# Kernel tuning notes

Hardware: AMD Instinct MI355X
Metric: run time of the kernel (lower is better)

The kernel has to match this reference:

```python
import jax, jax.numpy as jnp
import numpy as np
from jax import lax

ALPHA = 0.5
KERNEL = 25
NUM_P = 16
SEQ_LEN = 1440
PRED_LEN = 720
DWT_LEN = SEQ_LEN // 2 + 2            # 722 (pytorch_wavelets zero-mode, sym3 filt len 6)
FREQ = int(np.ceil(DWT_LEN / 2 * ALPHA) * 2)  # 362

_DEC_LO = np.array([0.035226291882100656, -0.08544127388224149, -0.13501102001039084,
                    0.4598775021193313, 0.8068915093133388, 0.3326705529509569], np.float32)
_DEC_HI = np.array([-0.3326705529509569, 0.8068915093133388, -0.4598775021193313,
                    -0.13501102001039084, 0.08544127388224149, 0.035226291882100656], np.float32)
DEC_LO, DEC_HI = jnp.asarray(_DEC_LO), jnp.asarray(_DEC_HI)
REC_LO, REC_HI = DEC_LO[::-1], DEC_HI[::-1]


def dwt1(x):
    # pytorch_wavelets DWT1DForward(J=1, mode='zero'): zero-pad then stride-2 true conv with dec filters
    B, C, L = x.shape
    out = (L + 5) // 2
    p = 2 * (out - 1) - L + 6
    xp = jnp.pad(x.reshape(B * C, 1, L), ((0, 0), (0, 0), (p // 2, p - p // 2)))
    ker = jnp.stack([DEC_LO[::-1], DEC_HI[::-1]])[:, None, :]   # (2,1,6); xcorr w/ reversed == conv
    y = lax.conv_general_dilated(xp, ker, (2,), 'VALID', dimension_numbers=('NCH', 'OIH', 'NCH'))
    return y[:, 0].reshape(B, C, out), y[:, 1].reshape(B, C, out)


def iwt1(lo, hi):
    # DWT1DInverse mode='zero': conv_transpose stride 2, padding L-2  ->  dilate + conv, pad 1
    B, C, n = lo.shape
    z = jnp.concatenate([lo.reshape(B * C, 1, n), hi.reshape(B * C, 1, n)], axis=1)
    ker = jnp.stack([REC_LO[::-1], REC_HI[::-1]])[None, :, :]   # (O=1, I=2, 6)
    y = lax.conv_general_dilated(z, ker, (1,), [(1, 1)], lhs_dilation=(2,),
                                 dimension_numbers=('NCH', 'OIH', 'NCH'))
    return y[:, 0].reshape(B, C, 2 * n - 4)


def mov_avg(x, k=KERNEL):
    pooled = lax.reduce_window(x, 0.0, lax.add, (1, 1, k), (1, 1, 1), 'VALID') / k
    return jnp.pad(pooled, ((0, 0), (0, 0), (k // 2, k // 2 - (k + 1) % 2)), mode='edge')


def mov_norm(x):
    mean = lax.stop_gradient(mov_avg(x))
    xc = lax.stop_gradient(x - mean)
    std = lax.stop_gradient(mov_avg(jnp.abs(xc))) + 1e-5
    return xc / std, mean, std


def inst_norm(x):
    mean = lax.stop_gradient(jnp.mean(x, -1, keepdims=True))
    xc = x - mean
    var = jnp.mean((xc - jnp.mean(xc, -1, keepdims=True)) ** 2, -1, keepdims=True)
    return xc / jnp.sqrt(var + 1e-5)


def mean_std_mlp(mean, std, mp, sp, mw1, mw2, sw1, sw2, mpred, spred):
    m_all = jnp.mean(mean, -1, keepdims=True)
    s_all = jnp.mean(std, -1, keepdims=True)
    mr = (mean - m_all) @ mp.T
    sr = (std - s_all) @ sp.T
    mr = jax.nn.relu(mr @ mw1.T) @ mw2.T
    sr = jax.nn.relu(sr @ sw1.T) @ sw2.T
    mean_o = mr @ mpred.T + m_all
    std_o = jax.nn.relu(sr @ spred.T + s_all) + 1e-5
    return mean_o, std_o


def forward(x, latent_w, latent_b, acp, dcp):
    xt = jnp.swapaxes(x, -1, 1)                    # (B, C, L)
    ac0, dc0 = dwt1(xt)                            # (B, C, DWT_LEN)
    ac_n = inst_norm(ac0)
    ac, m_ac, s_ac = mov_norm(ac0)
    dc, m_dc, s_dc = mov_norm(dc0)
    m_ac, s_ac = mean_std_mlp(m_ac, s_ac, *acp)    # MLPs[-1]
    m_dc, s_dc = mean_std_mlp(m_dc, s_dc, *dcp)    # MLPs[0]
    dcF = jnp.fft.fft(dc)
    acF = jnp.fft.fft(ac_n)
    idx = jnp.argsort(-jnp.abs(acF), axis=-1)[..., :FREQ]
    amp = ALPHA * jnp.take_along_axis(acF, idx, -1) + (1.0 - ALPHA) * jnp.take_along_axis(dcF, idx, -1)
    B, C, _ = dcF.shape
    bi = jnp.arange(B)[:, None, None]
    ci = jnp.arange(C)[None, :, None]
    dcF = dcF.at[bi, ci, idx].set(amp)
    dc = jnp.real(jnp.fft.ifft(dcF))
    xr = iwt1(ac, dc)                              # (B, C, SEQ_LEN)
    mean = iwt1(m_ac, m_dc)                        # (B, C, PRED_LEN)
    std = iwt1(s_ac, s_dc)
    xr = xr.reshape(B, C, NUM_P, SEQ_LEN // NUM_P)
    emb = xr @ latent_w.T + latent_b               # (B, C, NUM_P, d_model)
    return emb, mean, std


def setup_inputs() -> dict:
    key = jax.random.key(0)
    B, C = 64, 128
    d_model, d_ff = 512, 1024
    s = 0.02
    names_shapes = [
        ('x', (B, SEQ_LEN, C), 1.0),
        ('latent_w', (d_model, SEQ_LEN // NUM_P), s),
    ]
    for pre in ('ac', 'dc'):
        names_shapes += [
            (pre + '_mean_proj', (d_model, DWT_LEN), s),
            (pre + '_std_proj', (d_model, DWT_LEN), s),
            (pre + '_mean_ffn_w1', (d_ff, d_model), s),
            (pre + '_mean_ffn_w2', (d_model, d_ff), s),
            (pre + '_std_ffn_w1', (d_ff, d_model), s),
            (pre + '_std_ffn_w2', (d_model, d_ff), s),
            (pre + '_mean_pred', (PRED_LEN // 2 + 2, d_model), s),
            (pre + '_std_pred', (PRED_LEN // 2 + 2, d_model), s),
        ]
    keys = jax.random.split(key, len(names_shapes))
    inp = {n: jax.random.normal(k, shp, dtype=jnp.float32) * sc
           for (n, shp, sc), k in zip(names_shapes, keys)}
    inp['latent_b'] = jnp.zeros((d_model,), jnp.float32)
    return inp


def reference(x, latent_w, latent_b,
              ac_mean_proj, ac_std_proj, ac_mean_ffn_w1, ac_mean_ffn_w2,
              ac_std_ffn_w1, ac_std_ffn_w2, ac_mean_pred, ac_std_pred,
              dc_mean_proj, dc_std_proj, dc_mean_ffn_w1, dc_mean_ffn_w2,
              dc_std_ffn_w1, dc_std_ffn_w2, dc_mean_pred, dc_std_pred):
    acp = (ac_mean_proj, ac_std_proj, ac_mean_ffn_w1, ac_mean_ffn_w2,
           ac_std_ffn_w1, ac_std_ffn_w2, ac_mean_pred, ac_std_pred)
    dcp = (dc_mean_proj, dc_std_proj, dc_mean_ffn_w1, dc_mean_ffn_w2,
           dc_std_ffn_w1, dc_std_ffn_w2, dc_mean_pred, dc_std_pred)
    return forward(x, latent_w, latent_b, acp, dcp)
```

## Files before the change

kernel.cpp:

```cpp
#include <hip/hip_runtime.h>
#include <cmath>

#define RTOT 8192
#define NDWT 722
#define KP1  736
#define LSEQ 1440
#define NHEAD 362
#define NFREQ 362

typedef __bf16 bf16x8 __attribute__((ext_vector_type(8)));
typedef float f32x4 __attribute__((ext_vector_type(4)));
typedef float f32x2 __attribute__((ext_vector_type(2)));

__device__ __forceinline__ unsigned short f2bf(float f) {
    unsigned u = __float_as_uint(f);
    u += 0x7fffu + ((u >> 16) & 1u);
    return (unsigned short)(u >> 16);
}
__device__ __forceinline__ float bf2f(unsigned short u) {
    return __uint_as_float(((unsigned)u) << 16);
}

__device__ __forceinline__ void cmac(f32x2& s, f32x2 a, f32x2 w) {
    asm("v_pk_fma_f32 %0, %1, %2, %0 op_sel:[0,0,0] op_sel_hi:[0,1,1]\n\t"
        "v_pk_fma_f32 %0, %1, %2, %0 op_sel:[1,1,0] op_sel_hi:[1,0,1] neg_lo:[0,1,0]"
        : "+v"(s) : "v"(a), "v"(w));
}
__device__ __forceinline__ void cmac2(f32x2& s, f32x2 u, f32x2 v, f32x2 w) {
    asm("v_pk_fma_f32 %0, %1, %3, %0 op_sel:[0,0,0] op_sel_hi:[1,0,1]\n\t"
        "v_pk_fma_f32 %0, %2, %3, %0 op_sel:[1,1,0] op_sel_hi:[0,1,1] neg_lo:[0,1,0]"
        : "+v"(s) : "v"(u), "v"(v), "v"(w));
}
__device__ __forceinline__ f32x2 cmul(f32x2 a, f32x2 b) {
    f32x2 r;
    asm("v_pk_mul_f32 %0, %1, %2 op_sel:[0,0] op_sel_hi:[0,1]\n\t"
        "v_pk_fma_f32 %0, %1, %2, %0 op_sel:[1,1,0] op_sel_hi:[1,0,1] neg_lo:[0,1,0]"
        : "=&v"(r) : "v"(a), "v"(b));
    return r;
}

__constant__ float c_lo[6] = {0.035226291882100656f, -0.08544127388224149f, -0.13501102001039084f,
                              0.4598775021193313f, 0.8068915093133388f, 0.3326705529509569f};
__constant__ float c_hi[6] = {-0.3326705529509569f, 0.8068915093133388f, -0.4598775021193313f,
                              -0.13501102001039084f, 0.08544127388224149f, 0.035226291882100656f};

struct CvtDesc { const float* src; unsigned short* dst; int N, K, Np, Kp; };
struct CvtArgs { CvtDesc d[17]; float2* wtab; };
__global__ __launch_bounds__(256) void cvt_all_kernel(CvtArgs a) {
    if (blockIdx.y == 17) {
        int m = blockIdx.x * 256 + threadIdx.x;
        if (m < NDWT) {
            double ang = -2.0 * 3.141592653589793238462643383279502884 * (double)m / (double)NDWT;
            a.wtab[m] = make_float2((float)cos(ang), (float)sin(ang));
        }
        return;
    }
    CvtDesc d = a.d[blockIdx.y];
    int idx = blockIdx.x * 256 + threadIdx.x;
    int tot = d.Np * d.Kp;
    if (idx >= tot) return;
    int r = idx / d.Kp, c = idx - r * d.Kp;
    float v = (r < d.N && c < d.K) ? d.src[(size_t)r * d.K + c] : 0.f;
    d.dst[idx] = f2bf(v);
}

__global__ __launch_bounds__(256) void dwt_kernel(const float* __restrict__ x,
                                                  float* __restrict__ ac0,
                                                  float* __restrict__ dc0) {
    __shared__ float xs[68][129];
    const int b = blockIdx.x;
    const int t0 = blockIdx.y * 32;
    const int tid = threadIdx.x;
    const int lbase = 2 * t0 - 4;
    for (int i = tid; i < 68 * 32; i += 256) {
        int ri = i >> 5;
        int c4 = (i & 31) * 4;
        int l = lbase + ri;
        float4 v = make_float4(0.f, 0.f, 0.f, 0.f);
        if (l >= 0 && l < LSEQ)
            v = *reinterpret_cast<const float4*>(&x[((size_t)b * LSEQ + l) * 128 + c4]);
        xs[ri][c4] = v.x; xs[ri][c4 + 1] = v.y; xs[ri][c4 + 2] = v.z; xs[ri][c4 + 3] = v.w;
    }
    __syncthreads();
    const int tt = tid & 31;
    const int t = t0 + tt;
    const int cw = tid >> 5;
    if (t < NDWT) {
        #pragma unroll 4
        for (int co = 0; co < 16; co++) {
            int c = co * 8 + cw;
            float slo = 0.f, shi = 0.f;
            #pragma unroll
            for (int j = 0; j < 6; j++) {
                float v = xs[2 * tt + 5 - j][c];
                slo += v * c_lo[j];
                shi += v * c_hi[j];
            }
            size_t o = ((size_t)b * 128 + c) * NDWT + t;
            ac0[o] = slo;
            dc0[o] = shi;
        }
    }
}

__device__ __forceinline__ float blockSum256(float v, float* red) {
    #pragma unroll
    for (int o = 32; o > 0; o >>= 1) v += __shfl_down(v, o, 64);
    int lane = threadIdx.x & 63, wid = threadIdx.x >> 6;
    __syncthreads();
    if (lane == 0) red[wid] = v;
    __syncthreads();
    return red[0] + red[1] + red[2] + red[3];
}

template <bool ABS>
__device__ __forceinline__ void pool25(const float* rowv, float* pool, int tid) {
    int i0 = tid * 3;
    if (i0 < 698) {
        float s25 = 0.f;
        #pragma unroll
        for (int j = 0; j < 25; j++) { float v = rowv[i0 + j]; s25 += ABS ? fabsf(v) : v; }
        pool[i0] = s25 * (1.f / 25.f);
        #pragma unroll
        for (int qq = 1; qq < 3; qq++) {
            int i = i0 + qq;
            if (i < 698) {
                float vin = rowv[i + 24], vout = rowv[i - 1];
                s25 += (ABS ? fabsf(vin) : vin) - (ABS ? fabsf(vout) : vout);
                pool[i] = s25 * (1.f / 25.f);
            }
        }
    }
}

__global__ __launch_bounds__(256) void rowstats_kernel(
    const float* __restrict__ ac0in, const float* __restrict__ dc0in,
    float* __restrict__ acn,
    float* __restrict__ acp,
    float* __restrict__ dcp,
    unsigned short* __restrict__ cent,
    float* __restrict__ stat) {
    __shared__ float row[NDWT];
    __shared__ float xc[NDWT];
    __shared__ float pool[698];
    __shared__ float red[4];
    const int r = blockIdx.x, tid = threadIdx.x;
    const size_t base = (size_t)r * NDWT;
    const size_t baseP = (size_t)r * KP1;
    const size_t CS = (size_t)RTOT * KP1;

    if (blockIdx.y == 0) {
        for (int i = tid; i < NDWT; i += 256) row[i] = ac0in[base + i];
        __syncthreads();
        float s = 0.f;
        for (int i = tid; i < NDWT; i += 256) s += row[i];
        float mean = blockSum256(s, red) * (1.f / 722.f);
        s = 0.f;
        for (int i = tid; i < NDWT; i += 256) s += row[i] - mean;
        float m2 = blockSum256(s, red) * (1.f / 722.f);
        s = 0.f;
        for (int i = tid; i < NDWT; i += 256) { float d = row[i] - mean - m2; s += d * d; }
        float var = blockSum256(s, red) * (1.f / 722.f);
        float inv = 1.f / sqrtf(var + 1e-5f);
        for (int i = tid; i < NDWT; i += 256) acn[base + i] = (row[i] - mean) * inv;

        pool25<false>(row, pool, tid);
        __syncthreads();
        float msum = 0.f;
        for (int l = tid; l < NDWT; l += 256) {
            int pi = l - 12; pi = pi < 0 ? 0 : (pi > 697 ? 697 : pi);
            float m = pool[pi];
            msum += m;
            xc[l] = row[l] - m;
        }
        float m_all = blockSum256(msum, red) * (1.f / 722.f);
        __syncthreads();
        pool25<true>(xc, pool, tid);
        __syncthreads();
        float ssum = 0.f;
        for (int l = tid; l < NDWT; l += 256) {
            int pi = l - 12; pi = pi < 0 ? 0 : (pi > 697 ? 697 : pi);
            float sd = pool[pi] + 1e-5f;
            ssum += sd;
            acp[base + l] = xc[l] / sd;
        }
        float s_all = blockSum256(ssum, red) * (1.f / 722.f);
        if (tid == 0) { stat[r] = m_all; stat[RTOT + r] = s_all; }
        for (int l = tid; l < KP1; l += 256) {
            if (l < NDWT) {
                float m = row[l] - xc[l];
                int pi = l - 12; pi = pi < 0 ? 0 : (pi > 697 ? 697 : pi);
                float sd = pool[pi] + 1e-5f;
                cent[baseP + l]      = f2bf(m - m_all);
                cent[CS + baseP + l] = f2bf(sd - s_all);
            } else { cent[baseP + l] = 0; cent[CS + baseP + l] = 0; }
        }
    } else {
        for (int i = tid; i < NDWT; i += 256) row[i] = dc0in[base + i];
        __syncthreads();
        pool25<false>(row, pool, tid);
        __syncthreads();
        float msum2 = 0.f;
        for (int l = tid; l < NDWT; l += 256) {
            int pi = l - 12; pi = pi < 0 ? 0 : (pi > 697 ? 697 : pi);
            float m = pool[pi];
            msum2 += m;
            xc[l] = row[l] - m;
        }
        float m_all2 = blockSum256(msum2, red) * (1.f / 722.f);
        __syncthreads();
        pool25<true>(xc, pool, tid);
        __syncthreads();
        float ssum2 = 0.f;
        for (int l = tid; l < NDWT; l += 256) {
            int pi = l - 12; pi = pi < 0 ? 0 : (pi > 697 ? 697 : pi);
            float sd = pool[pi] + 1e-5f;
            ssum2 += sd;
            dcp[base + l] = xc[l] / sd;
        }
        float s_all2 = blockSum256(ssum2, red) * (1.f / 722.f);
        if (tid == 0) { stat[2 * RTOT + r] = m_all2; stat[3 * RTOT + r] = s_all2; }
        for (int l = tid; l < KP1; l += 256) {
            if (l < NDWT) {
                float m = row[l] - xc[l];
                int pi = l - 12; pi = pi < 0 ? 0 : (pi > 697 ? 697 : pi);
                float sd = pool[pi] + 1e-5f;
                cent[2 * CS + baseP + l] = f2bf(m - m_all2);
                cent[3 * CS + baseP + l] = f2bf(sd - s_all2);
            } else { cent[2 * CS + baseP + l] = 0; cent[3 * CS + baseP + l] = 0; }
        }
    }
}

__device__ void fft722_dev(f32x2* X, f32x2* T, const f32x2* Wt, const f32x2* W19) {
    const int tid = threadIdx.x;
    if (tid < 190) {
        const int c = tid / 38;
        const int g = tid - c * 38;
        const int p = (g >= 19) ? 1 : 0;
        const int rr = g - 19 * p;
        const int t0 = c * 4;
        const int nt = (c == 4) ? 3 : 4;
        const f32x2* xp = X + 2 * rr + p;
        f32x2 st[4], w[4], s[4];
        f32x2 a0 = xp[0];
        #pragma unroll
        for (int i = 0; i < 4; i++) {
            int ti = t0 + i; if (ti > 18) ti = 0;
            st[i] = W19[ti];
            w[i] = st[i];
            s[i] = a0;
        }
        #pragma unroll
        for (int m = 1; m <= 9; m++) {
            f32x2 a = xp[38 * m];
            f32x2 b = xp[38 * (19 - m)];
            f32x2 u = a + b, v = a - b;
            #pragma unroll
            for (int i = 0; i < 4; i++) {
                cmac2(s[i], u, v, w[i]);
                if (m < 9) w[i] = cmul(w[i], st[i]);
            }
        }
        int m0 = rr * t0;
        f32x2* Tp = T + p * 361 + rr * 19 + t0;
        #pragma unroll
        for (int i = 0; i < 4; i++) {
            if (i < nt) Tp[i] = cmul(s[i], Wt[2 * m0]);
            m0 += rr;
        }
    }
    __syncthreads();
    if (tid < 190) {
        const int c = tid / 38;
        const int g = tid - c * 38;
        const int p = (g >= 19) ? 1 : 0;
        const int t = g - 19 * p;
        const int jj0 = c * 4;
        const int nj = (c == 4) ? 3 : 4;
        const f32x2* Ap = T + p * 361 + t;
        f32x2 st[4], w[4], s[4];
        f32x2 a0 = Ap[0];
        #pragma unroll
        for (int i = 0; i < 4; i++) {
            int jj = jj0 + i; if (jj > 18) jj = 0;
            st[i] = W19[jj];
            w[i] = st[i];
            s[i] = a0;
        }
        #pragma unroll
        for (int m = 1; m <= 9; m++) {
            f32x2 a = Ap[19 * m];
            f32x2 b = Ap[19 * (19 - m)];
            f32x2 u = a + b, v = a - b;
            #pragma unroll
            for (int i = 0; i < 4; i++) {
                cmac2(s[i], u, v, w[i]);
                if (m < 9) w[i] = cmul(w[i], st[i]);
            }
        }
        f32x2* Xp = X + p * 361;
        #pragma unroll
        for (int i = 0; i < 4; i++) {
            int jj = jj0 + i;
            if (i < nj) Xp[t + 19 * jj] = s[i];
        }
    }
    __syncthreads();
    for (int k = tid; k < 361; k += 256) {
        f32x2 e = X[k], o = X[361 + k], w = Wt[k];
        f32x2 tt = {0.f, 0.f};
        cmac(tt, o, w);
        X[k] = e + tt;
        X[361 + k] = e - tt;
    }
    __syncthreads();
}

__global__ __launch_bounds__(256) void fft_mix_kernel(const float* __restrict__ acn,
                                                      float* __restrict__ dcp,
                                                      const f32x2* __restrict__ Wtab) {
    __shared__ f32x2 Wt[NDWT];
    __shared__ f32x2 W19s[19];
    __shared__ f32x2 B1[NDWT];
    __shared__ f32x2 B2[NDWT];
    __shared__ float smag[NDWT];
    __shared__ unsigned hist[256];
    __shared__ unsigned suf[256];
    __shared__ unsigned sh_digit, sh_rem;
    const int r = blockIdx.x, tid = threadIdx.x;
    const size_t base = (size_t)r * NDWT;

    for (int i = tid; i < NDWT; i += 256) Wt[i] = Wtab[i];
    if (tid < 19) W19s[tid] = Wtab[38 * tid];
    for (int i = tid; i < NDWT; i += 256) B1[i] = f32x2{acn[base + i], dcp[base + i]};
    __syncthreads();
    fft722_dev(B1, B2, Wt, W19s);
    for (int k = tid; k < 362; k += 256) {
        int m = (NDWT - k) % NDWT;
        f32x2 zk = B1[k], zm = B1[m];
        f32x2 ak = {0.5f * (zk.x + zm.x), 0.5f * (zk.y - zm.y)};
        f32x2 dk = {0.5f * (zk.y + zm.y), 0.5f * (zm.x - zk.x)};
        B1[k] = ak; B2[k] = dk;
        smag[k] = ak.x * ak.x + ak.y * ak.y;
        if (m != k) {
            f32x2 am = {0.5f * (zm.x + zk.x), 0.5f * (zm.y - zk.y)};
            f32x2 dm = {0.5f * (zm.y + zk.y), 0.5f * (zk.x - zm.x)};
            B1[m] = am; B2[m] = dm;
            smag[m] = am.x * am.x + am.y * am.y;
        }
    }
    __syncthreads();

    unsigned prefix = 0, rem = NFREQ;
    for (int shift = 24; shift >= 0; shift -= 8) {
        hist[tid] = 0;
        __syncthreads();
        unsigned hm = (shift == 24) ? 0u : (0xFFFFFFFFu << (shift + 8));
        for (int i = tid; i < NDWT; i += 256) {
            unsigned b = __float_as_uint(smag[i]);
            if ((b & hm) == prefix) atomicAdd(&hist[(b >> shift) & 255], 1u);
        }
        __syncthreads();
        suf[tid] = hist[tid];
        __syncthreads();
        for (int off = 1; off < 256; off <<= 1) {
            unsigned v = (tid + off < 256) ? suf[tid + off] : 0;
            __syncthreads();
            suf[tid] += v;
            __syncthreads();
        }
        unsigned Shere = suf[tid];
        unsigned Snext = (tid < 255) ? suf[tid + 1] : 0;
        if (Shere >= rem && Snext < rem) { sh_digit = (unsigned)tid; sh_rem = rem - Snext; }
        __syncthreads();
        prefix |= (sh_digit << shift);
        rem = sh_rem;
        __syncthreads();
    }
    int c0 = tid * 3, cnt = 0;
    #pragma unroll
    for (int j = 0; j < 3; j++) {
        int i = c0 + j;
        if (i < NDWT && __float_as_uint(smag[i]) == prefix) cnt++;
    }
    suf[tid] = (unsigned)cnt;
    __syncthreads();
    for (int off = 1; off < 256; off <<= 1) {
        unsigned v = (tid >= off) ? suf[tid - off] : 0;
        __syncthreads();
        suf[tid] += v;
        __syncthreads();
    }
    int myexc = (int)suf[tid] - cnt, o = 0;
    #pragma unroll
    for (int j = 0; j < 3; j++) {
        int i = c0 + j;
        if (i < NDWT) {
            unsigned b = __float_as_uint(smag[i]);
            int f = (b > prefix) ? 1 : 0;
            if (b == prefix) { if ((unsigned)(myexc + o) < rem) f = 1; o++; }
            smag[i] = f ? 1.f : 0.f;
        }
    }
    __syncthreads();

    for (int i = tid; i < NDWT; i += 256) {
        f32x2 d = B2[i];
        if (smag[i] != 0.f) { f32x2 a = B1[i]; d.x = 0.5f * (a.x + d.x); d.y = 0.5f * (a.y + d.y); }
        B1[i] = f32x2{d.x, -d.y};
    }
    __syncthreads();
    fft722_dev(B1, B2, Wt, W19s);
    for (int i = tid; i < NDWT; i += 256) dcp[base + i] = B1[i].x * (1.f / 722.f);
}

__global__ __launch_bounds__(256) void iwt_all_kernel(const unsigned short* __restrict__ heads,
                                                      const float* __restrict__ lo,
                                                      const float* __restrict__ hi,
                                                      float* __restrict__ out_mean,
                                                      float* __restrict__ out_std,
                                                      unsigned short* __restrict__ xrbf) {
    const int r = blockIdx.x;
    const int y = blockIdx.y;
    if (y < 6) {
        const int z = y / 3;
        const int t = (y % 3) * 256 + threadIdx.x;
        if (t >= 720) return;
        const size_t HR = (size_t)RTOT * NHEAD;
        const unsigned short* lp = heads + (size_t)z * HR + (size_t)r * NHEAD;
        const unsigned short* hp = heads + (size_t)(2 + z) * HR + (size_t)r * NHEAD;
        float* out = (z ? out_std : out_mean) + (size_t)r * 720;
        float s = 0.f;
        if (t & 1) {
            int j0 = (t - 1) >> 1;
            #pragma unroll
            for (int i = 0; i < 3; i++) s += bf2f(lp[j0 + i]) * c_lo[2 * i] + bf2f(hp[j0 + i]) * c_hi[2 * i];
        } else {
            int j0 = t >> 1;
            #pragma unroll
            for (int i = 0; i < 3; i++) s += bf2f(lp[j0 + i]) * c_lo[2 * i + 1] + bf2f(hp[j0 + i]) * c_hi[2 * i + 1];
        }
        out[t] = s;
    } else {
        const int yy = y - 6;
        const int t = yy * 256 + threadIdx.x;
        if (yy == 0 && threadIdx.x < 96) {
            int sub = threadIdx.x / 6, c = 90 + threadIdx.x % 6;
            xrbf[((size_t)r * 16 + sub) * 96 + c] = 0;
        }
        if (t >= LSEQ) return;
        const float* lp = lo + (size_t)r * NDWT;
        const float* hp = hi + (size_t)r * NDWT;
        float s = 0.f;
        if (t & 1) {
            int j0 = (t - 1) >> 1;
            #pragma unroll
            for (int i = 0; i < 3; i++) s += lp[j0 + i] * c_lo[2 * i] + hp[j0 + i] * c_hi[2 * i];
        } else {
            int j0 = t >> 1;
            #pragma unroll
            for (int i = 0; i < 3; i++) s += lp[j0 + i] * c_lo[2 * i + 1] + hp[j0 + i] * c_hi[2 * i + 1];
        }
        xrbf[((size_t)r * 16 + t / 90) * 96 + (t % 90)] = f2bf(s);
    }
}

struct ZPtrs { const unsigned short* p[4]; };
template <int EPI>
__global__ __launch_bounds__(256) void mfma_gemm_z(
    const unsigned short* __restrict__ A, int lda, size_t zsA,
    ZPtrs Wz, int ldw,
    void* __restrict__ Cout, int ldc, size_t zsC, int Nc,
    const float* __restrict__ biasBase, const float* __restrict__ cbias,
    int Ksteps) {
    __shared__ unsigned short As[2][128 * 32];
    __shared__ unsigned short Bs[2][128 * 32];
    const int z = blockIdx.z;
    const unsigned short* Az = A + (size_t)z * zsA;
    const unsigned short* W = Wz.p[z];
    const int tid = threadIdx.x;
    const int lane = tid & 63, wid = tid >> 6;
    const int bm = blockIdx.x * 128, bn = blockIdx.y * 128;
    const int wr = (wid >> 1) * 64, wc = (wid & 1) * 64;
    f32x4 acc[4][4] = {};
    const int srow = (lane >> 2);
    const int scol = (lane & 3) * 8;
    const int ch0 = wid * 2, ch1 = wid * 2 + 1;
    const unsigned short* ga0 = Az + (size_t)(bm + ch0 * 16 + srow) * lda + scol;
    const unsigned short* ga1 = Az + (size_t)(bm + ch1 * 16 + srow) * lda + scol;
    const unsigned short* gb0 = W + (size_t)(bn + ch0 * 16 + srow) * ldw + scol;
    const unsigned short* gb1 = W + (size_t)(bn + ch1 * 16 + srow) * ldw + scol;

#define STAGE_GL(buf, ks) do { const int k0_ = (ks) * 32;                                      \
    __builtin_amdgcn_global_load_lds((const __attribute__((address_space(1))) unsigned int*)(ga0 + k0_), \
        (__attribute__((address_space(3))) unsigned int*)(&As[buf][ch0 * 512]), 16, 0, 0);     \
    __builtin_amdgcn_global_load_lds((const __attribute__((address_space(1))) unsigned int*)(gb0 + k0_), \
        (__attribute__((address_space(3))) unsigned int*)(&Bs[buf][ch0 * 512]), 16, 0, 0);     \
    __builtin_amdgcn_global_load_lds((const __attribute__((address_space(1))) unsigned int*)(ga1 + k0_), \
        (__attribute__((address_space(3))) unsigned int*)(&As[buf][ch1 * 512]), 16, 0, 0);     \
    __builtin_amdgcn_global_load_lds((const __attribute__((address_space(1))) unsigned int*)(gb1 + k0_), \
        (__attribute__((address_space(3))) unsigned int*)(&Bs[buf][ch1 * 512]), 16, 0, 0);     \
    } while (0)

    STAGE_GL(0, 0);
    int cur = 0;
    const int kof = (lane >> 4) * 8;
    for (int ks = 0; ks < Ksteps; ks++) {
        if (ks + 1 < Ksteps) {
            STAGE_GL(cur ^ 1, ks + 1);
            asm volatile("s_waitcnt vmcnt(4)" ::: "memory");
        } else {
            asm volatile("s_waitcnt vmcnt(0)" ::: "memory");
        }
        __builtin_amdgcn_s_barrier();
        __builtin_amdgcn_sched_barrier(0);
        bf16x8 af[4], bfr[4];
        #pragma unroll
        for (int m = 0; m < 4; m++)
            af[m] = *reinterpret_cast<const bf16x8*>(&As[cur][(wr + m * 16 + (lane & 15)) * 32 + kof]);
        #pragma unroll
        for (int n = 0; n < 4; n++)
            bfr[n] = *reinterpret_cast<const bf16x8*>(&Bs[cur][(wc + n * 16 + (lane & 15)) * 32 + kof]);
        #pragma unroll
        for (int m = 0; m < 4; m++)
            #pragma unroll
            for (int n = 0; n < 4; n++)
                acc[m][n] = __builtin_amdgcn_mfma_f32_16x16x32_bf16(af[m], bfr[n], acc[m][n], 0, 0, 0);
        __builtin_amdgcn_s_barrier();
        __builtin_amdgcn_sched_barrier(0);
        cur ^= 1;
    }
#undef STAGE_GL

    unsigned short* Cb = (unsigned short*)Cout + (size_t)z * zsC;
    float* Cf = (float*)Cout + (size_t)z * zsC;
    const int crow0 = bm + wr + (lane >> 4) * 4;
    const int ccol0 = bn + wc + (lane & 15);
    #pragma unroll
    for (int m = 0; m < 4; m++) {
        #pragma unroll
        for (int n = 0; n < 4; n++) {
            const int col = ccol0 + n * 16;
            if (col < Nc) {
                #pragma unroll
                for (int q = 0; q < 4; q++) {
                    const int row = crow0 + m * 16 + q;
                    float v = acc[m][n][q];
                    if (EPI == 0) {
                        Cb[(size_t)row * ldc + col] = f2bf(v);
                    } else if (EPI == 1) {
                        Cb[(size_t)row * ldc + col] = f2bf(fmaxf(v, 0.f));
                    } else if (EPI == 4) {
                        Cf[(size_t)row * ldc + col] = v + cbias[col];
                    } else {
                        float ob = biasBase[(size_t)z * RTOT + row];
                        if (z & 1) v = fmaxf(v + ob, 0.f) + 1e-5f;
                        else       v += ob;
                        Cb[(size_t)row * ldc + col] = f2bf(v);
                    }
                }
            }
        }
    }
}

extern "C" void kernel_launch(void* const* d_in, const int* in_sizes, int n_in,
                              void* d_out, int out_size, void* d_ws, size_t ws_size,
                              hipStream_t stream) {
    const float* x = (const float*)d_in[0];
    const float* latent_w = (const float*)d_in[1];
    int p0;
    const float* latent_b;
    if (n_in > 2 && in_sizes[2] == 512) { latent_b = (const float*)d_in[2]; p0 = 3; }
    else                                { latent_b = (const float*)d_in[18]; p0 = 2; }

    char* wp = (char*)d_ws;
    auto alloc = [&](size_t bytes) { char* p = wp; wp += (bytes + 255) & ~(size_t)255; return p; };
    const size_t RN = (size_t)RTOT * NDWT;
    float* acn  = (float*)alloc(RN * 4);
    float* dcb  = (float*)alloc(RN * 4);
    float* acp  = (float*)alloc(RN * 4);
    float* stat = (float*)alloc(4 * RTOT * 4);
    float2* Wtab = (float2*)alloc(NDWT * 8);
    unsigned short* cent  = (unsigned short*)alloc((size_t)4 * RTOT * KP1 * 2);
    unsigned short* mlpB4 = (unsigned short*)alloc((size_t)4 * RTOT * 512 * 2);
    unsigned short* mlpA4 = (unsigned short*)alloc((size_t)4 * RTOT * 1024 * 2);
    unsigned short* mlpC4 = (unsigned short*)alloc((size_t)4 * RTOT * 512 * 2);
    unsigned short* heads = mlpB4;
    unsigned short* xrbf = mlpC4;
    unsigned short *projW[4], *w1W[4], *w2W[4], *predW[4];
    for (int z = 0; z < 4; z++) {
        projW[z] = (unsigned short*)alloc((size_t)512 * KP1 * 2);
        w1W[z]   = (unsigned short*)alloc((size_t)1024 * 512 * 2);
        w2W[z]   = (unsigned short*)alloc((size_t)512 * 1024 * 2);
        predW[z] = (unsigned short*)alloc((size_t)384 * 512 * 2);
    }
    unsigned short* latwb = (unsigned short*)alloc((size_t)512 * 96 * 2);
    (void)ws_size;

    CvtArgs ca;
    int si = 0;
    for (int z = 0; z < 4; z++) {
        int branch = z >> 1, isStd = z & 1, wb = p0 + branch * 8;
        ca.d[si++] = {(const float*)d_in[wb + isStd],         projW[z], 512, NDWT, 512, KP1};
        ca.d[si++] = {(const float*)d_in[wb + 2 + 2 * isStd], w1W[z], 1024, 512, 1024, 512};
        ca.d[si++] = {(const float*)d_in[wb + 3 + 2 * isStd], w2W[z], 512, 1024, 512, 1024};
        ca.d[si++] = {(const float*)d_in[wb + 6 + isStd],     predW[z], NHEAD, 512, 384, 512};
    }
    ca.d[16] = {latent_w, latwb, 512, 90, 512, 96};
    ca.wtab = Wtab;
    cvt_all_kernel<<<dim3(2048, 18), dim3(256), 0, stream>>>(ca);

    dwt_kernel<<<dim3(64, 23), dim3(256), 0, stream>>>(x, acn, dcb);
    rowstats_kernel<<<dim3(RTOT, 2), dim3(256), 0, stream>>>(acn, dcb, acn, acp, dcb, cent, stat);
    fft_mix_kernel<<<dim3(RTOT), dim3(256), 0, stream>>>(acn, dcb, (const f32x2*)Wtab);

    ZPtrs Zp = {{projW[0], projW[1], projW[2], projW[3]}};
    ZPtrs Z1 = {{w1W[0], w1W[1], w1W[2], w1W[3]}};
    ZPtrs Z2 = {{w2W[0], w2W[1], w2W[2], w2W[3]}};
    ZPtrs Zh = {{predW[0], predW[1], predW[2], predW[3]}};
    mfma_gemm_z<0><<<dim3(64, 4, 4), dim3(256), 0, stream>>>(
        cent, KP1, (size_t)RTOT * KP1, Zp, KP1, mlpB4, 512, (size_t)RTOT * 512, 512, nullptr, nullptr, KP1 / 32);
    mfma_gemm_z<1><<<dim3(64, 8, 4), dim3(256), 0, stream>>>(
        mlpB4, 512, (size_t)RTOT * 512, Z1, 512, mlpA4, 1024, (size_t)RTOT * 1024, 1024, nullptr, nullptr, 16);
    mfma_gemm_z<0><<<dim3(64, 4, 4), dim3(256), 0, stream>>>(
        mlpA4, 1024, (size_t)RTOT * 1024, Z2, 1024, mlpC4, 512, (size_t)RTOT * 512, 512, nullptr, nullptr, 32);
    mfma_gemm_z<5><<<dim3(64, 3, 4), dim3(256), 0, stream>>>(
        mlpC4, 512, (size_t)RTOT * 512, Zh, 512, heads, NHEAD, (size_t)RTOT * NHEAD, NHEAD, stat, nullptr, 16);

    float* out = (float*)d_out;
    float* out_mean = out + (size_t)67108864;
    float* out_std  = out_mean + (size_t)5898240;
    iwt_all_kernel<<<dim3(RTOT, 12), dim3(256), 0, stream>>>(heads, acp, dcb, out_mean, out_std, xrbf);

    ZPtrs Zl = {{latwb, latwb, latwb, latwb}};
    mfma_gemm_z<4><<<dim3(1024, 4, 1), dim3(256), 0, stream>>>(
        xrbf, 96, 0, Zl, 96, out, 512, 0, 512, nullptr, latent_b, 3);
}
```

Before: 523.9 us.

## Fuse row statistics kernel into FFT mixing kernel with shared LDS arena

Merges rowstats_kernel and fft_mix_kernel into one kernel per row. The instance-normalized ac row and the moving-normalized dc row are written straight into the FFT input buffer in LDS, so they are no longer stored to and reloaded from global memory. An aliased LDS arena keeps shared memory usage low. The risk is that each block now handles both branches serially, where before they ran as two parallel blocks, so per-block latency grows and there are fewer blocks in flight.

```diff
diff --git a/kernel.cpp b/kernel.cpp
--- a/kernel.cpp
+++ b/kernel.cpp
@@ -133,105 +133,6 @@
     }
 }
 
-__global__ __launch_bounds__(256) void rowstats_kernel(
-    const float* __restrict__ ac0in, const float* __restrict__ dc0in,
-    float* __restrict__ acn,
-    float* __restrict__ acp,
-    float* __restrict__ dcp,
-    unsigned short* __restrict__ cent,
-    float* __restrict__ stat) {
-    __shared__ float row[NDWT];
-    __shared__ float xc[NDWT];
-    __shared__ float pool[698];
-    __shared__ float red[4];
-    const int r = blockIdx.x, tid = threadIdx.x;
-    const size_t base = (size_t)r * NDWT;
-    const size_t baseP = (size_t)r * KP1;
-    const size_t CS = (size_t)RTOT * KP1;
-
-    if (blockIdx.y == 0) {
-        for (int i = tid; i < NDWT; i += 256) row[i] = ac0in[base + i];
-        __syncthreads();
-        float s = 0.f;
-        for (int i = tid; i < NDWT; i += 256) s += row[i];
-        float mean = blockSum256(s, red) * (1.f / 722.f);
-        s = 0.f;
-        for (int i = tid; i < NDWT; i += 256) s += row[i] - mean;
-        float m2 = blockSum256(s, red) * (1.f / 722.f);
-        s = 0.f;
-        for (int i = tid; i < NDWT; i += 256) { float d = row[i] - mean - m2; s += d * d; }
-        float var = blockSum256(s, red) * (1.f / 722.f);
-        float inv = 1.f / sqrtf(var + 1e-5f);
-        for (int i = tid; i < NDWT; i += 256) acn[base + i] = (row[i] - mean) * inv;
-
-        pool25<false>(row, pool, tid);
-        __syncthreads();
-        float msum = 0.f;
-        for (int l = tid; l < NDWT; l += 256) {
-            int pi = l - 12; pi = pi < 0 ? 0 : (pi > 697 ? 697 : pi);
-            float m = pool[pi];
-            msum += m;
-            xc[l] = row[l] - m;
-        }
-        float m_all = blockSum256(msum, red) * (1.f / 722.f);
-        __syncthreads();
-        pool25<true>(xc, pool, tid);
-        __syncthreads();
-        float ssum = 0.f;
-        for (int l = tid; l < NDWT; l += 256) {
-            int pi = l - 12; pi = pi < 0 ? 0 : (pi > 697 ? 697 : pi);
-            float sd = pool[pi] + 1e-5f;
-            ssum += sd;
-            acp[base + l] = xc[l] / sd;
-        }
-        float s_all = blockSum256(ssum, red) * (1.f / 722.f);
-        if (tid == 0) { stat[r] = m_all; stat[RTOT + r] = s_all; }
-        for (int l = tid; l < KP1; l += 256) {
-            if (l < NDWT) {
-                float m = row[l] - xc[l];
-                int pi = l - 12; pi = pi < 0 ? 0 : (pi > 697 ? 697 : pi);
-                float sd = pool[pi] + 1e-5f;
-                cent[baseP + l]      = f2bf(m - m_all);
-                cent[CS + baseP + l] = f2bf(sd - s_all);
-            } else { cent[baseP + l] = 0; cent[CS + baseP + l] = 0; }
-        }
-    } else {
-        for (int i = tid; i < NDWT; i += 256) row[i] = dc0in[base + i];
-        __syncthreads();
-        pool25<false>(row, pool, tid);
-        __syncthreads();
-        float msum2 = 0.f;
-        for (int l = tid; l < NDWT; l += 256) {
-            int pi = l - 12; pi = pi < 0 ? 0 : (pi > 697 ? 697 : pi);
-            float m = pool[pi];
-            msum2 += m;
-            xc[l] = row[l] - m;
-        }
-        float m_all2 = blockSum256(msum2, red) * (1.f / 722.f);
-        __syncthreads();
-        pool25<true>(xc, pool, tid);
-        __syncthreads();
-        float ssum2 = 0.f;
-        for (int l = tid; l < NDWT; l += 256) {
-            int pi = l - 12; pi = pi < 0 ? 0 : (pi > 697 ? 697 : pi);
-            float sd = pool[pi] + 1e-5f;
-            ssum2 += sd;
-            dcp[base + l] = xc[l] / sd;
-        }
-        float s_all2 = blockSum256(ssum2, red) * (1.f / 722.f);
-        if (tid == 0) { stat[2 * RTOT + r] = m_all2; stat[3 * RTOT + r] = s_all2; }
-        for (int l = tid; l < KP1; l += 256) {
-            if (l < NDWT) {
-                float m = row[l] - xc[l];
-                int pi = l - 12; pi = pi < 0 ? 0 : (pi > 697 ? 697 : pi);
-                float sd = pool[pi] + 1e-5f;
-                cent[2 * CS + baseP + l] = f2bf(m - m_all2);
-                cent[3 * CS + baseP + l] = f2bf(sd - s_all2);
-            } else { cent[2 * CS + baseP + l] = 0; cent[3 * CS + baseP + l] = 0; }
-        }
-    }
-}
-
 __device__ void fft722_dev(f32x2* X, f32x2* T, const f32x2* Wt, const f32x2* W19) {
     const int tid = threadIdx.x;
     if (tid < 190) {
@@ -317,24 +218,116 @@
     __syncthreads();
 }
 
-__global__ __launch_bounds__(256) void fft_mix_kernel(const float* __restrict__ acn,
-                                                      float* __restrict__ dcp,
-                                                      const f32x2* __restrict__ Wtab) {
+__global__ __launch_bounds__(256) void stats_fft_kernel(
+    const float* __restrict__ ac0in,
+    float* __restrict__ dcb,
+    float* __restrict__ acp,
+    unsigned short* __restrict__ cent,
+    float* __restrict__ stat,
+    const f32x2* __restrict__ Wtab) {
     __shared__ f32x2 Wt[NDWT];
     __shared__ f32x2 W19s[19];
     __shared__ f32x2 B1[NDWT];
-    __shared__ f32x2 B2[NDWT];
-    __shared__ float smag[NDWT];
+    __shared__ __align__(16) char arena[8704];
     __shared__ unsigned hist[256];
     __shared__ unsigned suf[256];
     __shared__ unsigned sh_digit, sh_rem;
+    f32x2* B2   = (f32x2*)arena;
+    float* smag = (float*)(arena + 5776);
+    float* row  = (float*)arena;
+    float* xc   = (float*)(arena + 2888);
+    float* pool = (float*)(arena + 5776);
+    float* red  = (float*)(arena + 8568);
     const int r = blockIdx.x, tid = threadIdx.x;
     const size_t base = (size_t)r * NDWT;
+    const size_t baseP = (size_t)r * KP1;
+    const size_t CS = (size_t)RTOT * KP1;
 
     for (int i = tid; i < NDWT; i += 256) Wt[i] = Wtab[i];
     if (tid < 19) W19s[tid] = Wtab[38 * tid];
-    for (int i = tid; i < NDWT; i += 256) B1[i] = f32x2{acn[base + i], dcp[base + i]};
-    __syncthreads();
+
+    for (int i = tid; i < NDWT; i += 256) row[i] = ac0in[base + i];
+    __syncthreads();
+    float s = 0.f;
+    for (int i = tid; i < NDWT; i += 256) s += row[i];
+    float mean = blockSum256(s, red) * (1.f / 722.f);
+    s = 0.f;
+    for (int i = tid; i < NDWT; i += 256) s += row[i] - mean;
+    float m2 = blockSum256(s, red) * (1.f / 722.f);
+    s = 0.f;
+    for (int i = tid; i < NDWT; i += 256) { float d = row[i] - mean - m2; s += d * d; }
+    float var = blockSum256(s, red) * (1.f / 722.f);
+    float inv = 1.f / sqrtf(var + 1e-5f);
+    for (int i = tid; i < NDWT; i += 256) B1[i].x = (row[i] - mean) * inv;
+
+    pool25<false>(row, pool, tid);
+    __syncthreads();
+    float msum = 0.f;
+    for (int l = tid; l < NDWT; l += 256) {
+        int pi = l - 12; pi = pi < 0 ? 0 : (pi > 697 ? 697 : pi);
+        float m = pool[pi];
+        msum += m;
+        xc[l] = row[l] - m;
+    }
+    float m_all = blockSum256(msum, red) * (1.f / 722.f);
+    __syncthreads();
+    pool25<true>(xc, pool, tid);
+    __syncthreads();
+    float ssum = 0.f;
+    for (int l = tid; l < NDWT; l += 256) {
+        int pi = l - 12; pi = pi < 0 ? 0 : (pi > 697 ? 697 : pi);
+        float sd = pool[pi] + 1e-5f;
+        ssum += sd;
+        acp[base + l] = xc[l] / sd;
+    }
+    float s_all = blockSum256(ssum, red) * (1.f / 722.f);
+    if (tid == 0) { stat[r] = m_all; stat[RTOT + r] = s_all; }
+    for (int l = tid; l < KP1; l += 256) {
+        if (l < NDWT) {
+            float m = row[l] - xc[l];
+            int pi = l - 12; pi = pi < 0 ? 0 : (pi > 697 ? 697 : pi);
+            float sd = pool[pi] + 1e-5f;
+            cent[baseP + l]      = f2bf(m - m_all);
+            cent[CS + baseP + l] = f2bf(sd - s_all);
+        } else { cent[baseP + l] = 0; cent[CS + baseP + l] = 0; }
+    }
+    __syncthreads();
+
+    for (int i = tid; i < NDWT; i += 256) row[i] = dcb[base + i];
+    __syncthreads();
+    pool25<false>(row, pool, tid);
+    __syncthreads();
+    float msum2 = 0.f;
+    for (int l = tid; l < NDWT; l += 256) {
+        int pi = l - 12; pi = pi < 0 ? 0 : (pi > 697 ? 697 : pi);
+        float m = pool[pi];
+        msum2 += m;
+        xc[l] = row[l] - m;
+    }
+    float m_all2 = blockSum256(msum2, red) * (1.f / 722.f);
+    __syncthreads();
+    pool25<true>(xc, pool, tid);
+    __syncthreads();
+    float ssum2 = 0.f;
+    for (int l = tid; l < NDWT; l += 256) {
+        int pi = l - 12; pi = pi < 0 ? 0 : (pi > 697 ? 697 : pi);
+        float sd = pool[pi] + 1e-5f;
+        ssum2 += sd;
+        B1[l].y = xc[l] / sd;
+    }
+    float s_all2 = blockSum256(ssum2, red) * (1.f / 722.f);
+    if (tid == 0) { stat[2 * RTOT + r] = m_all2; stat[3 * RTOT + r] = s_all2; }
+    for (int l = tid; l < KP1; l += 256) {
+        if (l < NDWT) {
+            float m = row[l] - xc[l];
+            int pi = l - 12; pi = pi < 0 ? 0 : (pi > 697 ? 697 : pi);
+            float sd = pool[pi] + 1e-5f;
+            cent[2 * CS + baseP + l] = f2bf(m - m_all2);
+            cent[3 * CS + baseP + l] = f2bf(sd - s_all2);
+        } else { cent[2 * CS + baseP + l] = 0; cent[3 * CS + baseP + l] = 0; }
+    }
+    __syncthreads();
+
     fft722_dev(B1, B2, Wt, W19s);
     for (int k = tid; k < 362; k += 256) {
         int m = (NDWT - k) % NDWT;
@@ -412,7 +405,7 @@
     }
     __syncthreads();
     fft722_dev(B1, B2, Wt, W19s);
-    for (int i = tid; i < NDWT; i += 256) dcp[base + i] = B1[i].x * (1.f / 722.f);
+    for (int i = tid; i < NDWT; i += 256) dcb[base + i] = B1[i].x * (1.f / 722.f);
 }
 
 __global__ __launch_bounds__(256) void iwt_all_kernel(const unsigned short* __restrict__ heads,
@@ -578,7 +571,7 @@
     char* wp = (char*)d_ws;
     auto alloc = [&](size_t bytes) { char* p = wp; wp += (bytes + 255) & ~(size_t)255; return p; };
     const size_t RN = (size_t)RTOT * NDWT;
-    float* acn  = (float*)alloc(RN * 4);
+    float* ac0b = (float*)alloc(RN * 4);
     float* dcb  = (float*)alloc(RN * 4);
     float* acp  = (float*)alloc(RN * 4);
     float* stat = (float*)alloc(4 * RTOT * 4);
@@ -612,9 +605,9 @@
     ca.wtab = Wtab;
     cvt_all_kernel<<<dim3(2048, 18), dim3(256), 0, stream>>>(ca);
 
-    dwt_kernel<<<dim3(64, 23), dim3(256), 0, stream>>>(x, acn, dcb);
-    rowstats_kernel<<<dim3(RTOT, 2), dim3(256), 0, stream>>>(acn, dcb, acn, acp, dcb, cent, stat);
-    fft_mix_kernel<<<dim3(RTOT), dim3(256), 0, stream>>>(acn, dcb, (const f32x2*)Wtab);
+    dwt_kernel<<<dim3(64, 23), dim3(256), 0, stream>>>(x, ac0b, dcb);
+    stats_fft_kernel<<<dim3(RTOT), dim3(256), 0, stream>>>(
+        ac0b, dcb, acp, cent, stat, (const f32x2*)Wtab);
 
     ZPtrs Zp = {{projW[0], projW[1], projW[2], projW[3]}};
     ZPtrs Z1 = {{w1W[0], w1W[1], w1W[2], w1W[3]}};
```

Result: no change. 523.3 us (-0.1%).
